# Performance work log

Hardware: AMD Instinct MI355X
Metric: run time of the kernel (lower is better)

Reference implementation:

```python
import jax, jax.numpy as jnp
import numpy as np

D, H = 8, 1024        # data_dim, hidden_size
ENC, HOR = 96, 336    # encode window, prediction horizon


def _cell(x, h, c, wih, whh, b):
    # PyTorch LSTM gate order: i, f, g, o
    g = x @ wih.T + h @ whh.T + b
    i, f, gg, o = jnp.split(g, 4, axis=-1)
    c2 = jax.nn.sigmoid(f) * c + jax.nn.sigmoid(i) * jnp.tanh(gg)
    h2 = jax.nn.sigmoid(o) * jnp.tanh(c2)
    return h2, c2


def _run_layer(xs, wih, whh, b, h0, c0):
    # xs: [T, B, in] -> outputs [T, B, out], final (h, c)
    def step(carry, xt):
        h, c = carry
        h2, c2 = _cell(xt, h, c, wih, whh, b)
        return (h2, c2), h2
    (hT, cT), hs = jax.lax.scan(step, (h0, c0), xs)
    return hs, hT, cT


def setup_inputs() -> dict:
    key = jax.random.key(0)
    ks = jax.random.split(key, 10)
    s = 1.0 / np.sqrt(H)
    inputs = jax.random.normal(ks[0], (64, ENC + HOR, D), dtype=jnp.float32)
    # lstm (2 layers, hidden H)
    w_ih0 = jax.random.normal(ks[1], (4 * H, D), dtype=jnp.float32) * s
    w_hh0 = jax.random.normal(ks[2], (4 * H, H), dtype=jnp.float32) * s
    b0 = jax.random.normal(ks[3], (4 * H,), dtype=jnp.float32) * s
    w_ih1 = jax.random.normal(ks[4], (4 * H, H), dtype=jnp.float32) * s
    w_hh1 = jax.random.normal(ks[5], (4 * H, H), dtype=jnp.float32) * s
    b1 = jax.random.normal(ks[6], (4 * H,), dtype=jnp.float32) * s
    # lstm2 (1 layer, hidden D)
    w_ih2 = jax.random.normal(ks[7], (4 * D, H), dtype=jnp.float32) * s
    w_hh2 = jax.random.normal(ks[8], (4 * D, D), dtype=jnp.float32) * s
    b2 = jax.random.normal(ks[9], (4 * D,), dtype=jnp.float32) * s
    return {"inputs": inputs, "w_ih0": w_ih0, "w_hh0": w_hh0, "b0": b0,
            "w_ih1": w_ih1, "w_hh1": w_hh1, "b1": b1,
            "w_ih2": w_ih2, "w_hh2": w_hh2, "b2": b2}


def reference(inputs, w_ih0, w_hh0, b0, w_ih1, w_hh1, b1, w_ih2, w_hh2, b2):
    x = inputs[..., :D]
    enc, y = x[:, :ENC], x[:, ENC:]          # [B,96,D], [B,336,D]
    B = enc.shape[0]
    zH = jnp.zeros((B, H), dtype=enc.dtype)
    zD = jnp.zeros((B, D), dtype=enc.dtype)

    # ---- encode: stacked LSTM over 96 steps ----
    xs = enc.transpose(1, 0, 2)              # [T,B,D]
    h1s, ha, ca = _run_layer(xs, w_ih0, w_hh0, b0, zH, zH)
    h2s, hb, cb = _run_layer(h1s, w_ih1, w_hh1, b1, zH, zH)
    hds, hd, cd = _run_layer(h2s, w_ih2, w_hh2, b2, zD, zD)
    pred0 = hds[-1]                          # [B,D]

    def dec(carry, _):
        p, ha, ca, hb, cb, hd, cd = carry
        ha, ca = _cell(p, ha, ca, w_ih0, w_hh0, b0)
        hb, cb = _cell(ha, hb, cb, w_ih1, w_hh1, b1)
        hd, cd = _cell(hb, hd, cd, w_ih2, w_hh2, b2)
        return (hd, ha, ca, hb, cb, hd, cd), hd

    _, preds = jax.lax.scan(dec, (pred0, ha, ca, hb, cb, hd, cd), None,
                            length=HOR - 1)  # [335,B,D]
    pred = jnp.concatenate([pred0[None], preds], axis=0).transpose(1, 0, 2)  # [B,336,D]
    loss = jnp.mean((pred - y) ** 2, axis=(0, 1))  # [D]
    return pred, y, loss
```

## Files before the change

### kernel.cpp

```cpp
#include <hip/hip_runtime.h>
#include <math.h>

#define B64 64
#define H 1024
#define DD 8
#define ENC 96
#define HOR 336
#define TT 432
#define NSTEP 431
#define NBLK 256
#define KS0 32
#define KS1 64

typedef __attribute__((ext_vector_type(8))) short short8;
typedef __attribute__((ext_vector_type(4))) float f32x4;
typedef unsigned long long ull;

__device__ __forceinline__ unsigned short f2bf(float x) {
    union { float f; unsigned u; } v; v.f = x;
    unsigned r = v.u + 0x7fffu + ((v.u >> 16) & 1u);
    return (unsigned short)(r >> 16);
}
__device__ __forceinline__ float sigm(float x) {
    return __builtin_amdgcn_rcpf(1.0f + __expf(-x));
}
__device__ __forceinline__ float ftanh(float x) {
    float e = __expf(fminf(x, 10.0f) * 2.0f);
    return (e - 1.0f) * __builtin_amdgcn_rcpf(e + 1.0f);
}

__device__ __forceinline__ short8 cload(const unsigned short* p) {
    const ull* q = (const ull*)p;
    ull lo = __hip_atomic_load(q,     __ATOMIC_RELAXED, __HIP_MEMORY_SCOPE_AGENT);
    ull hi = __hip_atomic_load(q + 1, __ATOMIC_RELAXED, __HIP_MEMORY_SCOPE_AGENT);
    union { ull u[2]; short8 s; } v; v.u[0] = lo; v.u[1] = hi;
    return v.s;
}
__device__ __forceinline__ void cstore8(ull* p, ull v) {
    __hip_atomic_store(p, v, __ATOMIC_RELAXED, __HIP_MEMORY_SCOPE_AGENT);
}


__global__ void zero_k(unsigned int* __restrict__ p, int n) {
    for (int i = blockIdx.x * 256 + threadIdx.x; i < n; i += gridDim.x * 256) p[i] = 0u;
}

__global__ void pack0_k(const float* __restrict__ w, unsigned short* __restrict__ dst) {
    const int total = 128 * 2 * KS0 * 64 * 8;
    for (int idx = blockIdx.x * 256 + threadIdx.x; idx < total; idx += gridDim.x * 256) {
        int j = idx & 7, lane = (idx >> 3) & 63, ks = (idx >> 9) & 31, nt = (idx >> 14) & 1, nb = idx >> 15;
        int rr = nt * 16 + (lane & 15);
        int row = nb * 8 + (rr >> 2) + 1024 * (rr & 3);
        int k = ks * 32 + ((lane >> 4) << 3) + j;
        dst[idx] = f2bf(w[row * 1024 + k]);
    }
}

__global__ void pack1_k(const float* __restrict__ wih, const float* __restrict__ whh,
                        unsigned short* __restrict__ dst) {
    const int total = 128 * 2 * KS1 * 64 * 8;
    for (int idx = blockIdx.x * 256 + threadIdx.x; idx < total; idx += gridDim.x * 256) {
        int j = idx & 7, lane = (idx >> 3) & 63, ks = (idx >> 9) & 63, nt = (idx >> 15) & 1, nb = idx >> 16;
        int rr = nt * 16 + (lane & 15);
        int row = nb * 8 + (rr >> 2) + 1024 * (rr & 3);
        int k = ks * 32 + ((lane >> 4) << 3) + j;
        float v = (k < 1024) ? wih[row * 1024 + k] : whh[row * 1024 + (k - 1024)];
        dst[idx] = f2bf(v);
    }
}

__global__ void pack2_k(const float* __restrict__ w, unsigned short* __restrict__ dst) {
    const int total = 2 * KS0 * 64 * 8;
    for (int idx = blockIdx.x * 256 + threadIdx.x; idx < total; idx += gridDim.x * 256) {
        int j = idx & 7, lane = (idx >> 3) & 63, ks = (idx >> 9) & 31, nt = (idx >> 14) & 1;
        int rr = nt * 16 + (lane & 15);
        int row = (rr >> 2) + 8 * (rr & 3);
        int k = ks * 32 + ((lane >> 4) << 3) + j;
        dst[idx] = f2bf(w[row * 1024 + k]);
    }
}

__global__ void copy_y_k(const float* __restrict__ inp, float* __restrict__ y) {
    const int total = B64 * HOR * DD;
    for (int i = blockIdx.x * 256 + threadIdx.x; i < total; i += gridDim.x * 256) {
        int b = i / (HOR * DD);
        int rem = i - b * (HOR * DD);
        y[i] = inp[b * (TT * DD) + ENC * DD + rem];
    }
}

__global__ void loss_k(const float* __restrict__ pred, const float* __restrict__ y,
                       float* __restrict__ loss) {
    __shared__ float part[256];
    int tid = threadIdx.x;
    int dd = tid & 7, cc = tid >> 3;
    float s = 0.f;
    for (int i = cc; i < B64 * HOR; i += 32) {
        float d = pred[i * 8 + dd] - y[i * 8 + dd];
        s += d * d;
    }
    part[tid] = s;
    __syncthreads();
    if (tid < 8) {
        float t = 0.f;
        for (int r = 0; r < 32; ++r) t += part[r * 8 + tid];
        loss[tid] = t / (float)(B64 * HOR);
    }
}

__device__ __forceinline__ void gbar_arrive(unsigned* dom, int rb, unsigned ep) {
    if (threadIdx.x == 0) {
        __builtin_amdgcn_s_waitcnt(0x0f70);
        __hip_atomic_store(dom + rb * 32, ep, __ATOMIC_RELAXED,
                           __HIP_MEMORY_SCOPE_AGENT);
    }
}
__device__ __forceinline__ void gbar_wait(unsigned* dom, unsigned ep) {
    const int tid = threadIdx.x;
    if (tid < 64) {
        const unsigned* f0 = dom + tid * 32;
        const unsigned* f1 = dom + (tid + 64) * 32;
        for (;;) {
            unsigned a = __hip_atomic_load(f0, __ATOMIC_RELAXED, __HIP_MEMORY_SCOPE_AGENT);
            unsigned b = __hip_atomic_load(f1, __ATOMIC_RELAXED, __HIP_MEMORY_SCOPE_AGENT);
            if (__all((a >= ep) && (b >= ep))) break;
        }
    }
    __syncthreads();
}

__global__ __launch_bounds__(256, 1) void persist_k(
    const unsigned short* __restrict__ Wp0,
    const unsigned short* __restrict__ Wp1,
    const unsigned short* __restrict__ Wp2,
    const float* __restrict__ wih0, const float* __restrict__ b0v,
    const float* __restrict__ b1v,
    const float* __restrict__ whh2, const float* __restrict__ b2v,
    const float* __restrict__ inp,
    unsigned short* __restrict__ H0a, unsigned short* __restrict__ H0b,
    unsigned short* __restrict__ H1a, unsigned short* __restrict__ H1b,
    unsigned* __restrict__ bar0, float* __restrict__ pred)
{
    const int tid = threadIdx.x;
    const int wv = tid >> 6, lane = tid & 63;
    const int blk = blockIdx.x;
    const int bg = blk & 1, rb = blk >> 1;
    const int bl = tid & 31, u = tid >> 5;
    const int mtl = bl >> 4, m16 = bl & 15;
    unsigned* dom = bar0 + (bg << 13);

    __shared__ float red1[16 * 272];
    __shared__ float red2[16 * 272];
    __shared__ float h2x[32 * 9];
    __shared__ ull hstage[32][2];

    for (int i = tid; i < 32 * 9; i += 256) h2x[i] = 0.f;

    short8 Wr0[2][8], Wr1h0[2][8], Wr1h1[2][8];
    {
        const short8* p0 = (const short8*)Wp0;
        const short8* p1 = (const short8*)Wp1;
        #pragma unroll
        for (int ot = 0; ot < 2; ++ot)
            #pragma unroll
            for (int kk = 0; kk < 8; ++kk) {
                Wr0[ot][kk]   = p0[((rb * 2 + ot) * KS0 + 8 * wv + kk) * 64 + lane];
                Wr1h0[ot][kk] = p1[((rb * 2 + ot) * KS1 + 8 * wv + kk) * 64 + lane];
                Wr1h1[ot][kk] = p1[((rb * 2 + ot) * KS1 + 32 + 8 * wv + kk) * 64 + lane];
            }
    }
    float wih0r[4][8], whh2r[4][8], b0r[4], b1r[4], b2r[4];
    #pragma unroll
    for (int g = 0; g < 4; ++g) {
        int row = rb * 8 + u + 1024 * g;
        #pragma unroll
        for (int d = 0; d < 8; ++d) wih0r[g][d] = wih0[row * 8 + d];
        b0r[g] = b0v[row];
        b1r[g] = b1v[row];
        int row2 = u + 8 * g;
        #pragma unroll
        for (int d = 0; d < 8; ++d) whh2r[g][d] = whh2[row2 * 8 + d];
        b2r[g] = b2v[row2];
    }
    float c0r = 0.f, c1r = 0.f, c2r = 0.f;
    unsigned ep = 0;

    auto redWrite = [&](float* red, f32x4 (&acc)[2][2]) {
        #pragma unroll
        for (int m = 0; m < 2; ++m)
            #pragma unroll
            for (int ot = 0; ot < 2; ++ot) {
                int base = ((wv * 2 + m) * 2 + ot) * 272 + (lane & 15) * 17 + (lane >> 4) * 4;
                #pragma unroll
                for (int r = 0; r < 4; ++r) red[base + r] = acc[m][ot][r];
            }
    };
    auto redSum = [&](const float* red, int g) {
        int rr = u * 4 + g, ot = rr >> 4, rr16 = rr & 15;
        float s = 0.f;
        #pragma unroll
        for (int w2i = 0; w2i < 4; ++w2i)
            s += red[((w2i * 2 + mtl) * 2 + ot) * 272 + rr16 * 17 + m16];
        return s;
    };
    auto hPublish = [&](unsigned short* Hw) {
        __syncthreads();
        if (tid < 32) {
            int b = bg * 32 + tid;
            int chunk = ((b >> 4) * KS0 + (rb >> 2)) * 64 + ((b & 15) | ((rb & 3) << 4));
            cstore8((ull*)Hw + chunk * 2,     hstage[tid][0]);
            cstore8((ull*)Hw + chunk * 2 + 1, hstage[tid][1]);
        }
    };

    short8 qa[8], qb[8];
    {
        union { ull u[2]; short8 s; } z; z.u[0] = 0; z.u[1] = 0;
        #pragma unroll
        for (int kk = 0; kk < 8; ++kk) { qa[kk] = z.s; qb[kk] = z.s; }
    }
    __syncthreads();

    {
        float xv[8];
        int b = bg * 32 + bl;
        #pragma unroll
        for (int d = 0; d < 8; ++d) xv[d] = inp[(b * TT + 0) * DD + d];
        float g4[4];
        #pragma unroll
        for (int g = 0; g < 4; ++g) {
            float s = b0r[g];
            #pragma unroll
            for (int d = 0; d < 8; ++d) s += wih0r[g][d] * xv[d];
            g4[g] = s;
        }
        c0r = sigm(g4[0]) * ftanh(g4[2]);
        float hn = sigm(g4[3]) * ftanh(c0r);
        ((unsigned short*)hstage)[bl * 8 + u] = f2bf(hn);
        hPublish(H0a);
    }
    gbar_arrive(dom, rb, ++ep);

    short8 pa[8], pb[8];

    for (int t = 0; t < NSTEP; ++t) {
        const int par = t & 1;
        const unsigned short* H0cur = par ? H0b : H0a;
        unsigned short* H1w = par ? H1b : H1a;
        unsigned short* H0nxt = par ? H0a : H0b;
        const bool last = (t == NSTEP - 1);

        f32x4 acc[2][2];
        #pragma unroll
        for (int m = 0; m < 2; ++m)
            #pragma unroll
            for (int ot = 0; ot < 2; ++ot) acc[m][ot] = (f32x4){0.f, 0.f, 0.f, 0.f};
        #pragma unroll
        for (int kk = 0; kk < 8; ++kk) {
            #pragma unroll
            for (int ot = 0; ot < 2; ++ot) {
                acc[0][ot] = __builtin_amdgcn_mfma_f32_16x16x32_bf16(qa[kk], Wr1h1[ot][kk], acc[0][ot], 0, 0, 0);
                acc[1][ot] = __builtin_amdgcn_mfma_f32_16x16x32_bf16(qb[kk], Wr1h1[ot][kk], acc[1][ot], 0, 0, 0);
            }
        }
        gbar_wait(dom, ep);

        {
            #pragma unroll
            for (int kk = 0; kk < 8; ++kk) {
                pa[kk] = cload(H0cur + (((bg * 2 + 0) * KS0 + 8 * wv + kk) * 64 + lane) * 8);
                pb[kk] = cload(H0cur + (((bg * 2 + 1) * KS0 + 8 * wv + kk) * 64 + lane) * 8);
            }
            #pragma unroll
            for (int kk = 0; kk < 8; ++kk) {
                #pragma unroll
                for (int ot = 0; ot < 2; ++ot) {
                    acc[0][ot] = __builtin_amdgcn_mfma_f32_16x16x32_bf16(pa[kk], Wr1h0[ot][kk], acc[0][ot], 0, 0, 0);
                    acc[1][ot] = __builtin_amdgcn_mfma_f32_16x16x32_bf16(pb[kk], Wr1h0[ot][kk], acc[1][ot], 0, 0, 0);
                }
            }
            redWrite(red1, acc);
            __syncthreads();
            float g4[4];
            #pragma unroll
            for (int g = 0; g < 4; ++g) g4[g] = b1r[g] + redSum(red1, g);
            c1r = sigm(g4[1]) * c1r + sigm(g4[0]) * ftanh(g4[2]);
            float hn = sigm(g4[3]) * ftanh(c1r);
            ((unsigned short*)hstage)[bl * 8 + u] = f2bf(hn);
            hPublish(H1w);
        }
        gbar_arrive(dom, rb, ++ep);

        short8 w2[2][8];
        {
            const short8* p2w = (const short8*)Wp2;
            #pragma unroll
            for (int ot = 0; ot < 2; ++ot)
                #pragma unroll
                for (int kk = 0; kk < 8; ++kk)
                    w2[ot][kk] = p2w[(ot * KS0 + 8 * wv + kk) * 64 + lane];
        }

        if (!last) {
            f32x4 a1[2][2];
            #pragma unroll
            for (int m = 0; m < 2; ++m)
                #pragma unroll
                for (int ot = 0; ot < 2; ++ot) a1[m][ot] = (f32x4){0.f, 0.f, 0.f, 0.f};
            #pragma unroll
            for (int kk = 0; kk < 8; ++kk) {
                #pragma unroll
                for (int ot = 0; ot < 2; ++ot) {
                    a1[0][ot] = __builtin_amdgcn_mfma_f32_16x16x32_bf16(pa[kk], Wr0[ot][kk], a1[0][ot], 0, 0, 0);
                    a1[1][ot] = __builtin_amdgcn_mfma_f32_16x16x32_bf16(pb[kk], Wr0[ot][kk], a1[1][ot], 0, 0, 0);
                }
            }
            redWrite(red2, a1);
        }
        gbar_wait(dom, ep);

        {
            #pragma unroll
            for (int kk = 0; kk < 8; ++kk) {
                qa[kk] = cload(H1w + (((bg * 2 + 0) * KS0 + 8 * wv + kk) * 64 + lane) * 8);
                qb[kk] = cload(H1w + (((bg * 2 + 1) * KS0 + 8 * wv + kk) * 64 + lane) * 8);
            }
            f32x4 a3[2][2];
            #pragma unroll
            for (int m = 0; m < 2; ++m)
                #pragma unroll
                for (int ot = 0; ot < 2; ++ot) a3[m][ot] = (f32x4){0.f, 0.f, 0.f, 0.f};
            #pragma unroll
            for (int kk = 0; kk < 8; ++kk) {
                #pragma unroll
                for (int ot = 0; ot < 2; ++ot) {
                    a3[0][ot] = __builtin_amdgcn_mfma_f32_16x16x32_bf16(qa[kk], w2[ot][kk], a3[0][ot], 0, 0, 0);
                    a3[1][ot] = __builtin_amdgcn_mfma_f32_16x16x32_bf16(qb[kk], w2[ot][kk], a3[1][ot], 0, 0, 0);
                }
            }
            redWrite(red1, a3);
            __syncthreads();
            float xo[8];
            #pragma unroll
            for (int d = 0; d < 8; ++d) xo[d] = h2x[bl * 9 + d];
            float g4[4];
            #pragma unroll
            for (int g = 0; g < 4; ++g) {
                float s = b2r[g] + redSum(red1, g);
                #pragma unroll
                for (int d = 0; d < 8; ++d) s += whh2r[g][d] * xo[d];
                g4[g] = s;
            }
            float cn = sigm(g4[1]) * c2r + sigm(g4[0]) * ftanh(g4[2]);
            c2r = cn;
            float hn2 = sigm(g4[3]) * ftanh(cn);
            __syncthreads();
            h2x[bl * 9 + u] = hn2;
            if (rb == 0 && t >= ENC - 1)
                pred[((bg * 32 + bl) * HOR + (t - (ENC - 1))) * DD + u] = hn2;

            if (!last) {
                __syncthreads();
                const int tt = t + 1;
                float xv[8];
                if (tt < ENC) {
                    int b = bg * 32 + bl;
                    #pragma unroll
                    for (int d = 0; d < 8; ++d) xv[d] = inp[(b * TT + tt) * DD + d];
                } else {
                    #pragma unroll
                    for (int d = 0; d < 8; ++d) xv[d] = h2x[bl * 9 + d];
                }
                float g1[4];
                #pragma unroll
                for (int g = 0; g < 4; ++g) {
                    float s = b0r[g] + redSum(red2, g);
                    #pragma unroll
                    for (int d = 0; d < 8; ++d) s += wih0r[g][d] * xv[d];
                    g1[g] = s;
                }
                c0r = sigm(g1[1]) * c0r + sigm(g1[0]) * ftanh(g1[2]);
                float hn0 = sigm(g1[3]) * ftanh(c0r);
                ((unsigned short*)hstage)[bl * 8 + u] = f2bf(hn0);
                hPublish(H0nxt);
                gbar_arrive(dom, rb, ++ep);
            }
        }
    }
}


extern "C" void kernel_launch(void* const* d_in, const int* in_sizes, int n_in,
                              void* d_out, int out_size, void* d_ws, size_t ws_size,
                              hipStream_t stream)
{
    const float* inp  = (const float*)d_in[0];
    const float* wih0 = (const float*)d_in[1];
    const float* whh0 = (const float*)d_in[2];
    const float* b0v  = (const float*)d_in[3];
    const float* wih1 = (const float*)d_in[4];
    const float* whh1 = (const float*)d_in[5];
    const float* b1v  = (const float*)d_in[6];
    const float* wih2 = (const float*)d_in[7];
    const float* whh2 = (const float*)d_in[8];
    const float* b2v  = (const float*)d_in[9];
    float* out = (float*)d_out;

    char* base = (char*)d_ws;
    size_t off = 0;
    auto carve = [&](size_t bytes) -> void* {
        void* p = base + off;
        off += (bytes + 255) & ~((size_t)255);
        return p;
    };
    unsigned short* Wp0 = (unsigned short*)carve((size_t)128 * 2 * KS0 * 64 * 8 * 2);
    unsigned short* Wp1 = (unsigned short*)carve((size_t)128 * 2 * KS1 * 64 * 8 * 2);
    unsigned short* Wp2 = (unsigned short*)carve((size_t)2 * KS0 * 64 * 8 * 2);
    size_t state_off = off;
    unsigned short* H0a = (unsigned short*)carve(B64 * H * 2);
    unsigned short* H0b = (unsigned short*)carve(B64 * H * 2);
    unsigned short* H1a = (unsigned short*)carve(B64 * H * 2);
    unsigned short* H1b = (unsigned short*)carve(B64 * H * 2);
    unsigned* bar = (unsigned*)carve(2 * 8192 * 4);
    size_t state_bytes = off - state_off;
    if (off > ws_size) return;

    zero_k<<<64, 256, 0, stream>>>((unsigned int*)(base + state_off), (int)(state_bytes / 4));
    pack0_k<<<2048, 256, 0, stream>>>(whh0, Wp0);
    pack1_k<<<4096, 256, 0, stream>>>(wih1, whh1, Wp1);
    pack2_k<<<32, 256, 0, stream>>>(wih2, Wp2);
    copy_y_k<<<672, 256, 0, stream>>>(inp, out + 172032);

    persist_k<<<NBLK, 256, 0, stream>>>(Wp0, Wp1, Wp2, wih0, b0v, b1v, whh2, b2v,
                                        inp, H0a, H0b, H1a, H1b, bar, out);

    loss_k<<<1, 256, 0, stream>>>(out, out + 172032, out + 344064);
}
```

Baseline: 3.567 ms.

## Replace flag barriers with tagged hidden-state words polled directly by consumers

Drops the separate flag-array barrier (arrive and wait) and instead stores each bf16 hidden value next to a 16-bit step tag inside 32-bit words. Consumers spin on the hidden-state data itself until every tag matches the current step, so they no longer need to poll flags and then reload the data. This is meant to cut barrier round-trip latency per recurrent step. In exchange the state buffers double in size, each poll reloads twice as many bytes, and the 16-bit tag is relied on to carry ordering, which depends on each 64-bit atomic store being seen as a single unit.

Result: slower. 8.717 ms (+144.4%).

```diff
diff --git a/kernel.cpp b/kernel.cpp
--- a/kernel.cpp
+++ b/kernel.cpp
@@ -29,12 +29,8 @@
     return (e - 1.0f) * __builtin_amdgcn_rcpf(e + 1.0f);
 }
 
-__device__ __forceinline__ short8 cload(const unsigned short* p) {
-    const ull* q = (const ull*)p;
-    ull lo = __hip_atomic_load(q,     __ATOMIC_RELAXED, __HIP_MEMORY_SCOPE_AGENT);
-    ull hi = __hip_atomic_load(q + 1, __ATOMIC_RELAXED, __HIP_MEMORY_SCOPE_AGENT);
-    union { ull u[2]; short8 s; } v; v.u[0] = lo; v.u[1] = hi;
-    return v.s;
+__device__ __forceinline__ ull cload8(const ull* p) {
+    return __hip_atomic_load(p, __ATOMIC_RELAXED, __HIP_MEMORY_SCOPE_AGENT);
 }
 __device__ __forceinline__ void cstore8(ull* p, ull v) {
     __hip_atomic_store(p, v, __ATOMIC_RELAXED, __HIP_MEMORY_SCOPE_AGENT);
@@ -108,27 +104,6 @@
     }
 }
 
-__device__ __forceinline__ void gbar_arrive(unsigned* dom, int rb, unsigned ep) {
-    if (threadIdx.x == 0) {
-        __builtin_amdgcn_s_waitcnt(0x0f70);
-        __hip_atomic_store(dom + rb * 32, ep, __ATOMIC_RELAXED,
-                           __HIP_MEMORY_SCOPE_AGENT);
-    }
-}
-__device__ __forceinline__ void gbar_wait(unsigned* dom, unsigned ep) {
-    const int tid = threadIdx.x;
-    if (tid < 64) {
-        const unsigned* f0 = dom + tid * 32;
-        const unsigned* f1 = dom + (tid + 64) * 32;
-        for (;;) {
-            unsigned a = __hip_atomic_load(f0, __ATOMIC_RELAXED, __HIP_MEMORY_SCOPE_AGENT);
-            unsigned b = __hip_atomic_load(f1, __ATOMIC_RELAXED, __HIP_MEMORY_SCOPE_AGENT);
-            if (__all((a >= ep) && (b >= ep))) break;
-        }
-    }
-    __syncthreads();
-}
-
 __global__ __launch_bounds__(256, 1) void persist_k(
     const unsigned short* __restrict__ Wp0,
     const unsigned short* __restrict__ Wp1,
@@ -137,9 +112,9 @@
     const float* __restrict__ b1v,
     const float* __restrict__ whh2, const float* __restrict__ b2v,
     const float* __restrict__ inp,
-    unsigned short* __restrict__ H0a, unsigned short* __restrict__ H0b,
-    unsigned short* __restrict__ H1a, unsigned short* __restrict__ H1b,
-    unsigned* __restrict__ bar0, float* __restrict__ pred)
+    unsigned* __restrict__ H0a, unsigned* __restrict__ H0b,
+    unsigned* __restrict__ H1a, unsigned* __restrict__ H1b,
+    float* __restrict__ pred)
 {
     const int tid = threadIdx.x;
     const int wv = tid >> 6, lane = tid & 63;
@@ -147,12 +122,11 @@
     const int bg = blk & 1, rb = blk >> 1;
     const int bl = tid & 31, u = tid >> 5;
     const int mtl = bl >> 4, m16 = bl & 15;
-    unsigned* dom = bar0 + (bg << 13);
 
     __shared__ float red1[16 * 272];
     __shared__ float red2[16 * 272];
     __shared__ float h2x[32 * 9];
-    __shared__ ull hstage[32][2];
+    __shared__ unsigned short hstage[32][8];
 
     for (int i = tid; i < 32 * 9; i += 256) h2x[i] = 0.f;
 
@@ -183,7 +157,6 @@
         b2r[g] = b2v[row2];
     }
     float c0r = 0.f, c1r = 0.f, c2r = 0.f;
-    unsigned ep = 0;
 
     auto redWrite = [&](float* red, f32x4 (&acc)[2][2]) {
         #pragma unroll
@@ -203,13 +176,54 @@
             s += red[((w2i * 2 + mtl) * 2 + ot) * 272 + rr16 * 17 + m16];
         return s;
     };
-    auto hPublish = [&](unsigned short* Hw) {
+    auto hPublish = [&](unsigned* Hw, unsigned tag) {
         __syncthreads();
         if (tid < 32) {
             int b = bg * 32 + tid;
             int chunk = ((b >> 4) * KS0 + (rb >> 2)) * 64 + ((b & 15) | ((rb & 3) << 4));
-            cstore8((ull*)Hw + chunk * 2,     hstage[tid][0]);
-            cstore8((ull*)Hw + chunk * 2 + 1, hstage[tid][1]);
+            const unsigned short* hs = &hstage[tid][0];
+            ull tg = ((ull)tag << 48) | ((ull)tag << 16);
+            ull* dst = (ull*)Hw + chunk * 4;
+            #pragma unroll
+            for (int jj = 0; jj < 4; ++jj) {
+                ull w = tg | (ull)hs[2 * jj] | ((ull)hs[2 * jj + 1] << 32);
+                cstore8(dst + jj, w);
+            }
+        }
+    };
+    auto hPoll = [&](const unsigned* Hw, unsigned tag, short8 (&fa)[8], short8 (&fb)[8]) {
+        const ull* src = (const ull*)Hw;
+        const ull tg2 = ((ull)tag << 48) | ((ull)tag << 16);
+        ull wa[32], wb[32];
+        for (;;) {
+            #pragma unroll
+            for (int kk = 0; kk < 8; ++kk) {
+                int ca = (((bg * 2 + 0) * KS0 + 8 * wv + kk) * 64 + lane) * 4;
+                int cb = (((bg * 2 + 1) * KS0 + 8 * wv + kk) * 64 + lane) * 4;
+                #pragma unroll
+                for (int jj = 0; jj < 4; ++jj) {
+                    wa[kk * 4 + jj] = cload8(src + ca + jj);
+                    wb[kk * 4 + jj] = cload8(src + cb + jj);
+                }
+            }
+            ull bad = 0;
+            #pragma unroll
+            for (int i = 0; i < 32; ++i) {
+                bad |= (wa[i] ^ tg2) & 0xFFFF0000FFFF0000ull;
+                bad |= (wb[i] ^ tg2) & 0xFFFF0000FFFF0000ull;
+            }
+            if (__all(bad == 0)) break;
+        }
+        #pragma unroll
+        for (int kk = 0; kk < 8; ++kk) {
+            #pragma unroll
+            for (int jj = 0; jj < 4; ++jj) {
+                ull a = wa[kk * 4 + jj], b = wb[kk * 4 + jj];
+                fa[kk][2 * jj]     = (short)(unsigned short)(a);
+                fa[kk][2 * jj + 1] = (short)(unsigned short)(a >> 32);
+                fb[kk][2 * jj]     = (short)(unsigned short)(b);
+                fb[kk][2 * jj + 1] = (short)(unsigned short)(b >> 32);
+            }
         }
     };
 
@@ -236,19 +250,19 @@
         }
         c0r = sigm(g4[0]) * ftanh(g4[2]);
         float hn = sigm(g4[3]) * ftanh(c0r);
-        ((unsigned short*)hstage)[bl * 8 + u] = f2bf(hn);
-        hPublish(H0a);
-    }
-    gbar_arrive(dom, rb, ++ep);
+        hstage[bl][u] = f2bf(hn);
+        hPublish(H0a, 1u);
+    }
 
     short8 pa[8], pb[8];
 
     for (int t = 0; t < NSTEP; ++t) {
         const int par = t & 1;
-        const unsigned short* H0cur = par ? H0b : H0a;
-        unsigned short* H1w = par ? H1b : H1a;
-        unsigned short* H0nxt = par ? H0a : H0b;
+        const unsigned* H0cur = par ? H0b : H0a;
+        unsigned* H1w = par ? H1b : H1a;
+        unsigned* H0nxt = par ? H0a : H0b;
         const bool last = (t == NSTEP - 1);
+        const unsigned tagc = (unsigned)t + 1;
 
         f32x4 acc[2][2];
         #pragma unroll
@@ -263,14 +277,9 @@
                 acc[1][ot] = __builtin_amdgcn_mfma_f32_16x16x32_bf16(qb[kk], Wr1h1[ot][kk], acc[1][ot], 0, 0, 0);
             }
         }
-        gbar_wait(dom, ep);
 
         {
-            #pragma unroll
-            for (int kk = 0; kk < 8; ++kk) {
-                pa[kk] = cload(H0cur + (((bg * 2 + 0) * KS0 + 8 * wv + kk) * 64 + lane) * 8);
-                pb[kk] = cload(H0cur + (((bg * 2 + 1) * KS0 + 8 * wv + kk) * 64 + lane) * 8);
-            }
+            hPoll(H0cur, tagc, pa, pb);
             #pragma unroll
             for (int kk = 0; kk < 8; ++kk) {
                 #pragma unroll
@@ -286,10 +295,9 @@
             for (int g = 0; g < 4; ++g) g4[g] = b1r[g] + redSum(red1, g);
             c1r = sigm(g4[1]) * c1r + sigm(g4[0]) * ftanh(g4[2]);
             float hn = sigm(g4[3]) * ftanh(c1r);
-            ((unsigned short*)hstage)[bl * 8 + u] = f2bf(hn);
-            hPublish(H1w);
-        }
-        gbar_arrive(dom, rb, ++ep);
+            hstage[bl][u] = f2bf(hn);
+            hPublish(H1w, tagc);
+        }
 
         short8 w2[2][8];
         {
@@ -317,14 +325,9 @@
             }
             redWrite(red2, a1);
         }
-        gbar_wait(dom, ep);
 
         {
-            #pragma unroll
-            for (int kk = 0; kk < 8; ++kk) {
-                qa[kk] = cload(H1w + (((bg * 2 + 0) * KS0 + 8 * wv + kk) * 64 + lane) * 8);
-                qb[kk] = cload(H1w + (((bg * 2 + 1) * KS0 + 8 * wv + kk) * 64 + lane) * 8);
-            }
+            hPoll(H1w, tagc, qa, qb);
             f32x4 a3[2][2];
             #pragma unroll
             for (int m = 0; m < 2; ++m)
@@ -381,9 +384,8 @@
                 }
                 c0r = sigm(g1[1]) * c0r + sigm(g1[0]) * ftanh(g1[2]);
                 float hn0 = sigm(g1[3]) * ftanh(c0r);
-                ((unsigned short*)hstage)[bl * 8 + u] = f2bf(hn0);
-                hPublish(H0nxt);
-                gbar_arrive(dom, rb, ++ep);
+                hstage[bl][u] = f2bf(hn0);
+                hPublish(H0nxt, tagc + 1u);
             }
         }
     }
@@ -417,11 +419,10 @@
     unsigned short* Wp1 = (unsigned short*)carve((size_t)128 * 2 * KS1 * 64 * 8 * 2);
     unsigned short* Wp2 = (unsigned short*)carve((size_t)2 * KS0 * 64 * 8 * 2);
     size_t state_off = off;
-    unsigned short* H0a = (unsigned short*)carve(B64 * H * 2);
-    unsigned short* H0b = (unsigned short*)carve(B64 * H * 2);
-    unsigned short* H1a = (unsigned short*)carve(B64 * H * 2);
-    unsigned short* H1b = (unsigned short*)carve(B64 * H * 2);
-    unsigned* bar = (unsigned*)carve(2 * 8192 * 4);
+    unsigned* H0a = (unsigned*)carve((size_t)B64 * H * 4);
+    unsigned* H0b = (unsigned*)carve((size_t)B64 * H * 4);
+    unsigned* H1a = (unsigned*)carve((size_t)B64 * H * 4);
+    unsigned* H1b = (unsigned*)carve((size_t)B64 * H * 4);
     size_t state_bytes = off - state_off;
     if (off > ws_size) return;
 
@@ -432,7 +433,7 @@
     copy_y_k<<<672, 256, 0, stream>>>(inp, out + 172032);
 
     persist_k<<<NBLK, 256, 0, stream>>>(Wp0, Wp1, Wp2, wih0, b0v, b1v, whh2, b2v,
-                                        inp, H0a, H0b, H1a, H1b, bar, out);
+                                        inp, H0a, H0b, H1a, H1b, out);
 
     loss_k<<<1, 256, 0, stream>>>(out, out + 172032, out + 344064);
 }
```
